# Kernel optimization log

Hardware: AMD Instinct MI355X
Metric: run time of the kernel (lower is better)

## Reference

```python
import jax, jax.numpy as jnp
import numpy as np

EPS = 1e-06
NUM_HEADS = 16
THETA = 10000.0


def rope_tables(grid_size, head_dim):
    # matches VisionRotaryEmbeddingFast: 2D rope, table shape [grid^2, head_dim]
    half = head_dim // 2
    freqs = 1.0 / THETA ** (jnp.arange(0, half, 2, dtype=jnp.float32) / half)
    freqs = jnp.concatenate([freqs, freqs], axis=0)  # [half]
    t = jnp.arange(grid_size, dtype=jnp.float32)
    f = jnp.outer(t, freqs)  # [grid, half]
    fh = jnp.broadcast_to(f[:, None, :], (grid_size, grid_size, half))
    fw = jnp.broadcast_to(f[None, :, :], (grid_size, grid_size, half))
    full = jnp.concatenate([fh, fw], axis=-1).reshape(-1, head_dim)  # [N, head_dim]
    return jnp.cos(full), jnp.sin(full)


def rotate_half(x):
    n = x.shape[-1] // 2
    return jnp.concatenate((-x[..., n:], x[..., :n]), axis=-1)


def rms_norm(x, gamma):
    var = jnp.mean(x * x, axis=-1, keepdims=True)
    return x * jax.lax.rsqrt(var + EPS) * gamma


def setup_inputs() -> dict:
    key = jax.random.key(0)
    ks = jax.random.split(key, 5)
    B, N, C = 32, 1024, 1024
    return {
        "x": jax.random.normal(ks[0], (B, N, C), dtype=jnp.float32),
        "qkv_w": jax.random.normal(ks[1], (C, 3 * C), dtype=jnp.float32) * (C ** -0.5),
        "qkv_b": jnp.zeros((3 * C,), dtype=jnp.float32),
        "proj_w": jax.random.normal(ks[2], (C, C), dtype=jnp.float32) * (C ** -0.5),
        "proj_b": jnp.zeros((C,), dtype=jnp.float32),
        "q_gamma": jnp.ones((C // NUM_HEADS,), dtype=jnp.float32),
        "k_gamma": jnp.ones((C // NUM_HEADS,), dtype=jnp.float32),
    }


def reference(x, qkv_w, qkv_b, proj_w, proj_b, q_gamma, k_gamma):
    B, N, C = x.shape
    H = NUM_HEADS
    hd = C // H
    grid = int(np.sqrt(N))
    cos, sin = rope_tables(grid, hd)  # [N, hd] each
    cos = cos[None, :, None, :]  # broadcast over [B, N, H, hd]
    sin = sin[None, :, None, :]

    qkv = (x @ qkv_w + qkv_b).reshape(B, N, 3, H, hd)
    q, k, v = qkv[:, :, 0], qkv[:, :, 1], qkv[:, :, 2]  # [B, N, H, hd]

    q = rms_norm(q, q_gamma)
    k = rms_norm(k, k_gamma)
    q = q * cos + rotate_half(q) * sin
    k = k * cos + rotate_half(k) * sin

    out = jax.nn.dot_product_attention(q, k, v, is_causal=False)  # [B, N, H, hd]
    out = out.reshape(B, N, C)
    return out @ proj_w + proj_b
```

## Files before the change

### kernel.cpp

```cpp
#include <hip/hip_runtime.h>
#include <stdint.h>

typedef float f32x4 __attribute__((ext_vector_type(4)));
typedef float f32x16 __attribute__((ext_vector_type(16)));
typedef short s16x8 __attribute__((ext_vector_type(8)));
typedef unsigned short u16;

__device__ __forceinline__ u16 f2bf(float f) {
  union { float f; uint32_t u; } c; c.f = f;
  uint32_t u = c.u;
  u = (u + 0x7fffu + ((u >> 16) & 1u)) >> 16;
  return (u16)u;
}

__device__ __forceinline__ void gload16(const void* g, void* lds) {
  __builtin_amdgcn_global_load_lds(
      (const __attribute__((address_space(1))) void*)g,
      (__attribute__((address_space(3))) void*)lds, 16, 0, 0);
}

__device__ __forceinline__ f32x4 mfma16(s16x8 a, s16x8 b, f32x4 c) {
  return __builtin_amdgcn_mfma_f32_16x16x32_bf16(a, b, c, 0, 0, 0);
}

__device__ __forceinline__ f32x16 mfma32(s16x8 a, s16x8 b, f32x16 c) {
  return __builtin_amdgcn_mfma_f32_32x32x16_bf16(a, b, c, 0, 0, 0);
}

__device__ __forceinline__ int swz(int row, int c8) {
  return row * 64 + ((c8 ^ (row & 7)) << 3);
}

__global__ void cvt_bf16(const float* __restrict__ in, u16* __restrict__ out, size_t n) {
  size_t i = ((size_t)blockIdx.x * blockDim.x + threadIdx.x) * 4;
  if (i < n) {
    float4 v = *(const float4*)&in[i];
    u16 o0 = f2bf(v.x), o1 = f2bf(v.y), o2 = f2bf(v.z), o3 = f2bf(v.w);
    uint2 packed;
    packed.x = (uint32_t)o0 | ((uint32_t)o1 << 16);
    packed.y = (uint32_t)o2 | ((uint32_t)o3 << 16);
    *(uint2*)&out[i] = packed;
  }
}

__global__ void transpose_cvt(const float* __restrict__ in, u16* __restrict__ out,
                              int rows, int cols) {
  __shared__ float tile[64][65];
  const int c0 = blockIdx.x * 64, r0 = blockIdx.y * 64;
  const int tr = threadIdx.x >> 6, tc = threadIdx.x & 63;
#pragma unroll
  for (int i = 0; i < 16; i++) {
    int r = i * 4 + tr;
    tile[r][tc] = in[(size_t)(r0 + r) * cols + c0 + tc];
  }
  __syncthreads();
#pragma unroll
  for (int i = 0; i < 16; i++) {
    int oc = i * 4 + tr;
    out[(size_t)(c0 + oc) * rows + r0 + tc] = f2bf(tile[tc][oc]);
  }
}

__global__ void rope_tables_kernel(float* __restrict__ cosT, float* __restrict__ sinT) {
  int n = blockIdx.x;
  int d = threadIdx.x;
  int ph = n >> 5, pw = n & 31;
  int pos = (d < 32) ? ph : pw;
  int fi = d & 15;
  float freq = powf(10000.f, -(float)fi / 16.f);
  float ang = (float)pos * freq;
  cosT[n * 64 + d] = cosf(ang);
  sinT[n * 64 + d] = sinf(ang);
}


#define PH_MID \
  __builtin_amdgcn_sched_barrier(0); \
  __builtin_amdgcn_s_barrier(); \
  asm volatile("s_waitcnt lgkmcnt(0)" ::: "memory"); \
  __builtin_amdgcn_sched_barrier(0); \
  __builtin_amdgcn_s_setprio(1);

#define PH_END \
  __builtin_amdgcn_s_setprio(0); \
  __builtin_amdgcn_sched_barrier(0); \
  __builtin_amdgcn_s_barrier(); \
  __builtin_amdgcn_sched_barrier(0);

#define STAGE(ldsoff, g) do { \
    gload16((g) + (size_t)(w8 + srow) * 1024 + sc8 * 8,       &lds[(ldsoff) + w8 * 64]); \
    gload16((g) + (size_t)(w8 + srow + 64) * 1024 + sc8 * 8,  &lds[(ldsoff) + (w8 + 64) * 64]); \
  } while (0)

#define RD_A(dst, BUF, mh) \
  _Pragma("unroll") \
  for (int mi = 0; mi < 4; mi++) { \
    dst[mi][0] = *(const s16x8*)&lds[(BUF) * 32768 + arow0 + ((mh) * 64 + mi * 16) * 64 + swz0]; \
    dst[mi][1] = *(const s16x8*)&lds[(BUF) * 32768 + arow0 + ((mh) * 64 + mi * 16) * 64 + swz1]; \
  }

#define RD_B(dst, BUF, nh) \
  _Pragma("unroll") \
  for (int ni = 0; ni < 2; ni++) { \
    dst[ni][0] = *(const s16x8*)&lds[(BUF) * 32768 + 16384 + brow0 + ((nh) * 32 + ni * 16) * 64 + swz0]; \
    dst[ni][1] = *(const s16x8*)&lds[(BUF) * 32768 + 16384 + brow0 + ((nh) * 32 + ni * 16) * 64 + swz1]; \
  }

#define MFMA_QUAD(af, bfr, mh, nh) \
  _Pragma("unroll") \
  for (int mi = 0; mi < 4; mi++) \
    _Pragma("unroll") \
    for (int ni = 0; ni < 2; ni++) { \
      acc[(mh) * 4 + mi][(nh) * 2 + ni] = mfma16(af[mi][0], bfr[ni][0], acc[(mh) * 4 + mi][(nh) * 2 + ni]); \
      acc[(mh) * 4 + mi][(nh) * 2 + ni] = mfma16(af[mi][1], bfr[ni][1], acc[(mh) * 4 + mi][(nh) * 2 + ni]); \
    }

#define KTILE(BUF, KT, MODE) do { \
    s16x8 a0f[4][2], a1f[4][2], b0f[2][2], b1f[2][2]; \
     \
    RD_A(a0f, BUF, 0); \
    RD_B(b0f, BUF, 0); \
    if ((MODE) < 2) STAGE((1 - (BUF)) * 32768, Ag + (size_t)((KT) + 1) * 64); \
    PH_MID; MFMA_QUAD(a0f, b0f, 0, 0); PH_END; \
     \
    RD_B(b1f, BUF, 1); \
    if ((MODE) < 2) STAGE((1 - (BUF)) * 32768 + 8192, Ag + (size_t)128 * 1024 + ((KT) + 1) * 64); \
    PH_MID; MFMA_QUAD(a0f, b1f, 0, 1); PH_END; \
     \
    RD_A(a1f, BUF, 1); \
    if ((MODE) == 0) STAGE((BUF) * 32768 + 16384, Bg + (size_t)((KT) + 2) * 64); \
    PH_MID; MFMA_QUAD(a1f, b1f, 1, 1); PH_END; \
     \
    if ((MODE) == 0) STAGE((BUF) * 32768 + 16384 + 8192, Bg + (size_t)128 * 1024 + ((KT) + 2) * 64); \
    PH_MID; MFMA_QUAD(a1f, b0f, 1, 0); \
    __builtin_amdgcn_s_setprio(0); \
    if ((MODE) == 0) asm volatile("s_waitcnt vmcnt(4)" ::: "memory"); \
    if ((MODE) == 1) asm volatile("s_waitcnt vmcnt(0)" ::: "memory"); \
    __builtin_amdgcn_sched_barrier(0); \
    __builtin_amdgcn_s_barrier(); \
    __builtin_amdgcn_sched_barrier(0); \
  } while (0)

__device__ __forceinline__ void gemm_mainloop_8ph(
    const u16* __restrict__ Ag, const u16* __restrict__ Bg,
    u16* lds, f32x4 (&acc)[8][4])
{
  const int t = threadIdx.x;
  const int l = t & 63, w = t >> 6;
  const int wm = w & 1, wn = w >> 1;
  const int lrow = l & 15, lg = l >> 4;
  const int srow = l >> 3, sc8 = (l & 7) ^ srow;
  const int w8 = w * 8;
  const int swz0 = ((0 + lg) ^ (lrow & 7)) << 3;
  const int swz1 = ((4 + lg) ^ (lrow & 7)) << 3;
  const int arow0 = (wm * 128 + lrow) * 64;
  const int brow0 = (wn * 64 + lrow) * 64;

  STAGE(0,                 Ag);
  STAGE(8192,              Ag + (size_t)128 * 1024);
  STAGE(16384,             Bg);
  STAGE(16384 + 8192,      Bg + (size_t)128 * 1024);
  STAGE(32768 + 16384,          Bg + 64);
  STAGE(32768 + 16384 + 8192,   Bg + (size_t)128 * 1024 + 64);
  asm volatile("s_waitcnt vmcnt(4)" ::: "memory");
  __builtin_amdgcn_sched_barrier(0);
  __builtin_amdgcn_s_barrier();
  __builtin_amdgcn_sched_barrier(0);

#pragma unroll 1
  for (int kt = 0; kt < 14; kt += 2) {
    KTILE(0, kt, 0);
    KTILE(1, kt + 1, 0);
  }
  KTILE(0, 14, 1);
  KTILE(1, 15, 2);
}

__global__ __launch_bounds__(512, 2) void gemm_qkv(
    const u16* __restrict__ A,
    const u16* __restrict__ Bt,
    const float* __restrict__ bias,
    const float* __restrict__ qgam, const float* __restrict__ kgam,
    const float* __restrict__ cosT, const float* __restrict__ sinT,
    u16* __restrict__ qb, u16* __restrict__ kb, u16* __restrict__ vb)
{
  __shared__ u16 lds[65536];
  const int bid = blockIdx.x;
  const int sb = (bid & 7) * 192 + (bid >> 3);
  const int bm = sb / 12, bn = sb % 12;

  const f32x4 fzero = {0.f, 0.f, 0.f, 0.f};
  f32x4 acc[8][4];
#pragma unroll
  for (int i = 0; i < 8; i++)
#pragma unroll
    for (int j = 0; j < 4; j++) acc[i][j] = fzero;

  gemm_mainloop_8ph(A + (size_t)bm * 256 * 1024, Bt + (size_t)bn * 256 * 1024, lds, acc);

  const int t = threadIdx.x, l = t & 63, w = t >> 6;
  const int wm = w & 1, wn = w >> 1, lrow = l & 15, lg = l >> 4;
  const int colb = bn * 256 + wn * 64;
  const int s = colb >> 10;
  const int h = (colb & 1023) >> 6;

  float biasv[4];
#pragma unroll
  for (int nt = 0; nt < 4; nt++) biasv[nt] = bias[colb + nt * 16 + lrow];

  if (s < 2) {
    u16* dst = (s == 0) ? qb : kb;
    const float mul = (s == 0) ? 0.18033688011112042f : 1.0f;
    const float* gamma = (s == 0) ? qgam : kgam;
    float g[4];
#pragma unroll
    for (int nt = 0; nt < 4; nt++) g[nt] = gamma[nt * 16 + lrow] * mul;
#pragma unroll
    for (int mf = 0; mf < 8; mf++) {
#pragma unroll
      for (int r = 0; r < 4; r++) {
        const int rowg = bm * 256 + wm * 128 + mf * 16 + lg * 4 + r;
        const int b = rowg >> 10, np = rowg & 1023;
        float tmp[4]; float sq = 0.f;
#pragma unroll
        for (int nt = 0; nt < 4; nt++) {
          float v = acc[mf][nt][r] + biasv[nt];
          tmp[nt] = v; sq += v * v;
        }
#pragma unroll
        for (int off = 1; off < 16; off <<= 1) sq += __shfl_xor(sq, off);
        const float rstd = rsqrtf(sq * 0.015625f + 1e-6f);
#pragma unroll
        for (int nt = 0; nt < 4; nt++) tmp[nt] *= rstd * g[nt];
        const size_t base = (((size_t)(b * 16 + h)) * 1024 + np) * 64;
#pragma unroll
        for (int nt = 0; nt < 4; nt++) {
          const int d = nt * 16 + lrow;
          const float cv = cosT[np * 64 + d], sv = sinT[np * 64 + d];
          const float rh = (nt < 2) ? -tmp[nt + 2] : tmp[nt - 2];
          dst[base + d] = f2bf(tmp[nt] * cv + rh * sv);
        }
      }
    }
  } else {
#pragma unroll
    for (int mf = 0; mf < 8; mf++) {
#pragma unroll
      for (int r = 0; r < 4; r++) {
        const int rowg = bm * 256 + wm * 128 + mf * 16 + lg * 4 + r;
        const int b = rowg >> 10, np = rowg & 1023;
        const size_t hb = ((size_t)(b * 16 + h)) * 64;
#pragma unroll
        for (int nt = 0; nt < 4; nt++) {
          const int d = nt * 16 + lrow;
          vb[(hb + d) * 1024 + np] = f2bf(acc[mf][nt][r] + biasv[nt]);
        }
      }
    }
  }
}

__global__ __launch_bounds__(256, 2) void attn_kernel(
    const u16* __restrict__ qbuf, const u16* __restrict__ kbuf,
    const u16* __restrict__ vtbuf, u16* __restrict__ obuf)
{
  __shared__ u16 Qs[256 * 64];
  __shared__ u16 Ks[2][64 * 64];
  __shared__ u16 VTs[2][64 * 64];
  __shared__ float lsumS[4][2][32];
  const int bx = blockIdx.x;
  const int xcd = bx & 7, idx = bx >> 3;
  const int bh = xcd * 64 + (idx >> 2), qt = idx & 3;
  const int t = threadIdx.x, l = t & 63, w = t >> 6;
  const int q31 = l & 31, hi = l >> 5;

  const u16* qg  = qbuf  + (size_t)bh * 65536 + (size_t)qt * 16384;
  const u16* kg0 = kbuf  + (size_t)bh * 65536;
  const u16* vt0 = vtbuf + (size_t)bh * 65536;

  const int srow = l >> 3;
  const int sc8  = (l & 7) ^ (srow & 7);

#pragma unroll
  for (int i = 0; i < 8; i++) {
    const int r0 = (w + i * 4) * 8;
    gload16(qg + (size_t)(r0 + srow) * 64 + sc8 * 8, &Qs[r0 * 64]);
  }
#pragma unroll
  for (int i = 0; i < 2; i++) {
    const int r0 = (w + i * 4) * 8;
    gload16(kg0 + (size_t)(r0 + srow) * 64 + sc8 * 8, &Ks[0][r0 * 64]);
    gload16(vt0 + (size_t)(r0 + srow) * 1024 + sc8 * 8, &VTs[0][r0 * 64]);
  }
  asm volatile("s_waitcnt vmcnt(0)" ::: "memory");
  __syncthreads();

  s16x8 bq[2][4];
#pragma unroll
  for (int qb = 0; qb < 2; qb++)
#pragma unroll
    for (int ds = 0; ds < 4; ds++)
      bq[qb][ds] = *(const s16x8*)&Qs[swz(w * 64 + qb * 32 + q31, ds * 2 + hi)];

  f32x16 o[2][2];
#pragma unroll
  for (int qb = 0; qb < 2; qb++)
#pragma unroll
    for (int kb2 = 0; kb2 < 2; kb2++)
#pragma unroll
      for (int i = 0; i < 16; i++) o[qb][kb2][i] = 0.f;
  float l_[2] = {0.f, 0.f};

#pragma unroll 2
  for (int kt = 0; kt < 16; kt++) {
    const int cur = kt & 1;
    if (kt < 15) {
      const int kb = (kt + 1) * 64;
#pragma unroll
      for (int i = 0; i < 2; i++) {
        const int r0 = (w + i * 4) * 8;
        gload16(kg0 + (size_t)(kb + r0 + srow) * 64 + sc8 * 8, &Ks[cur ^ 1][r0 * 64]);
        gload16(vt0 + (size_t)(r0 + srow) * 1024 + kb + sc8 * 8, &VTs[cur ^ 1][r0 * 64]);
      }
    }

    f32x16 s[2][2];
#pragma unroll
    for (int qb = 0; qb < 2; qb++)
#pragma unroll
      for (int kb2 = 0; kb2 < 2; kb2++)
#pragma unroll
        for (int i = 0; i < 16; i++) s[qb][kb2][i] = 0.f;
    __builtin_amdgcn_s_setprio(1);
#pragma unroll
    for (int ds = 0; ds < 4; ds++) {
      s16x8 ak0 = *(const s16x8*)&Ks[cur][swz(q31, ds * 2 + hi)];
      s16x8 ak1 = *(const s16x8*)&Ks[cur][swz(32 + q31, ds * 2 + hi)];
      s[0][0] = mfma32(ak0, bq[0][ds], s[0][0]);
      s[0][1] = mfma32(ak1, bq[0][ds], s[0][1]);
      s[1][0] = mfma32(ak0, bq[1][ds], s[1][0]);
      s[1][1] = mfma32(ak1, bq[1][ds], s[1][1]);
    }
    __builtin_amdgcn_s_setprio(0);

    s16x8 pf[2][4];
#pragma unroll
    for (int qb = 0; qb < 2; qb++) {
      float p[32];
#pragma unroll
      for (int r = 0; r < 16; r++) p[r] = __builtin_amdgcn_exp2f(s[qb][0][r]);
#pragma unroll
      for (int r = 0; r < 16; r++) p[16 + r] = __builtin_amdgcn_exp2f(s[qb][1][r]);
      {
        float sm0 = 0.f, sm1 = 0.f, sm2 = 0.f, sm3 = 0.f;
#pragma unroll
        for (int r = 0; r < 8; r++) {
          sm0 += p[r]; sm1 += p[8 + r]; sm2 += p[16 + r]; sm3 += p[24 + r];
        }
        l_[qb] += (sm0 + sm1) + (sm2 + sm3);
      }
#pragma unroll
      for (int j = 0; j < 4; j++) {
        uint32_t a1, b1, a2, b2;
        asm("v_cvt_pk_bf16_f32 %0, %1, %2" : "=v"(a1) : "v"(p[j * 8 + 0]), "v"(p[j * 8 + 1]));
        asm("v_cvt_pk_bf16_f32 %0, %1, %2" : "=v"(b1) : "v"(p[j * 8 + 2]), "v"(p[j * 8 + 3]));
        asm("v_cvt_pk_bf16_f32 %0, %1, %2" : "=v"(a2) : "v"(p[j * 8 + 4]), "v"(p[j * 8 + 5]));
        asm("v_cvt_pk_bf16_f32 %0, %1, %2" : "=v"(b2) : "v"(p[j * 8 + 6]), "v"(p[j * 8 + 7]));
        asm("v_permlane32_swap_b32 %0, %1" : "+v"(a1), "+v"(a2));
        asm("v_permlane32_swap_b32 %0, %1" : "+v"(b1), "+v"(b2));
        union { s16x8 v; uint32_t u[4]; } cvt;
        cvt.u[0] = a1; cvt.u[1] = b1; cvt.u[2] = a2; cvt.u[3] = b2;
        pf[qb][j] = cvt.v;
      }
    }

    __builtin_amdgcn_s_setprio(1);
#pragma unroll
    for (int j = 0; j < 4; j++) {
      s16x8 bv0 = *(const s16x8*)&VTs[cur][swz(q31, j * 2 + hi)];
      s16x8 bv1 = *(const s16x8*)&VTs[cur][swz(32 + q31, j * 2 + hi)];
      o[0][0] = mfma32(pf[0][j], bv0, o[0][0]);
      o[0][1] = mfma32(pf[0][j], bv1, o[0][1]);
      o[1][0] = mfma32(pf[1][j], bv0, o[1][0]);
      o[1][1] = mfma32(pf[1][j], bv1, o[1][1]);
    }
    __builtin_amdgcn_s_setprio(0);

    __syncthreads();
  }

#pragma unroll
  for (int qb = 0; qb < 2; qb++) {
    l_[qb] += __shfl_xor(l_[qb], 32);
    if (l < 32) lsumS[w][qb][q31] = 1.0f / l_[qb];
  }

  const int b = bh >> 4, h = bh & 15;
#pragma unroll
  for (int qb = 0; qb < 2; qb++)
#pragma unroll
    for (int r = 0; r < 16; r++) {
      const int q = (r & 3) + 8 * (r >> 2) + 4 * hi;
      const float inv = lsumS[w][qb][q];
      const int n = qt * 256 + w * 64 + qb * 32 + q;
      const size_t base = (((size_t)b * 1024 + n) * 16 + h) * 64;
      obuf[base + q31]      = f2bf(o[qb][0][r] * inv);
      obuf[base + 32 + q31] = f2bf(o[qb][1][r] * inv);
    }
}

__global__ __launch_bounds__(512, 2) void gemm_proj(
    const u16* __restrict__ A,
    const u16* __restrict__ Bt,
    const float* __restrict__ bias,
    float* __restrict__ out)
{
  __shared__ u16 lds[65536];
  const int bid = blockIdx.x;
  const int sb = (bid & 7) * 64 + (bid >> 3);
  const int bm = sb >> 2, bn = sb & 3;

  const f32x4 fzero = {0.f, 0.f, 0.f, 0.f};
  f32x4 acc[8][4];
#pragma unroll
  for (int i = 0; i < 8; i++)
#pragma unroll
    for (int j = 0; j < 4; j++) acc[i][j] = fzero;

  gemm_mainloop_8ph(A + (size_t)bm * 256 * 1024, Bt + (size_t)bn * 256 * 1024, lds, acc);

  const int t = threadIdx.x, l = t & 63, w = t >> 6;
  const int wm = w & 1, wn = w >> 1, lrow = l & 15, lg = l >> 4;
  const int colb = bn * 256 + wn * 64;
  float biasv[4];
#pragma unroll
  for (int nt = 0; nt < 4; nt++) biasv[nt] = bias[colb + nt * 16 + lrow];

#pragma unroll
  for (int mf = 0; mf < 8; mf++) {
#pragma unroll
    for (int r = 0; r < 4; r++) {
      const int rowg = bm * 256 + wm * 128 + mf * 16 + lg * 4 + r;
#pragma unroll
      for (int nt = 0; nt < 4; nt++) {
        const int col = colb + nt * 16 + lrow;
        out[(size_t)rowg * 1024 + col] = acc[mf][nt][r] + biasv[nt];
      }
    }
  }
}

extern "C" void kernel_launch(void* const* d_in, const int* in_sizes, int n_in,
                              void* d_out, int out_size, void* d_ws, size_t ws_size,
                              hipStream_t stream) {
  const float* x      = (const float*)d_in[0];
  const float* qkv_w  = (const float*)d_in[1];
  const float* qkv_b  = (const float*)d_in[2];
  const float* proj_w = (const float*)d_in[3];
  const float* proj_b = (const float*)d_in[4];
  const float* q_gam  = (const float*)d_in[5];
  const float* k_gam  = (const float*)d_in[6];

  char* ws = (char*)d_ws;
  u16*   xb   = (u16*)(ws);
  u16*   qb   = (u16*)(ws + 67108864);
  u16*   kb   = (u16*)(ws + 134217728);
  u16*   vb   = (u16*)(ws + 201326592);
  u16*   wqT  = (u16*)(ws + 268435456);
  u16*   wpT  = (u16*)(ws + 274726912);
  float* cosT = (float*)(ws + 276824064);
  float* sinT = (float*)(ws + 277086208);
  u16*   attn = xb;

  cvt_bf16<<<32768, 256, 0, stream>>>(x, xb, (size_t)33554432);
  transpose_cvt<<<dim3(48, 16), 256, 0, stream>>>(qkv_w, wqT, 1024, 3072);
  transpose_cvt<<<dim3(16, 16), 256, 0, stream>>>(proj_w, wpT, 1024, 1024);
  rope_tables_kernel<<<1024, 64, 0, stream>>>(cosT, sinT);

  gemm_qkv<<<dim3(1536), dim3(512), 0, stream>>>(xb, wqT, qkv_b, q_gam, k_gam,
                                                 cosT, sinT, qb, kb, vb);
  attn_kernel<<<2048, 256, 0, stream>>>(qb, kb, vb, attn);
  gemm_proj<<<dim3(512), dim3(512), 0, stream>>>(attn, wpT, proj_b, (float*)d_out);
}
```

Before: 685.1 us.

## Raise attention occupancy by dropping Q LDS tile and splitting KV tile in halves

```diff
diff --git a/kernel.cpp b/kernel.cpp
--- a/kernel.cpp
+++ b/kernel.cpp
@@ -260,11 +260,10 @@
   }
 }
 
-__global__ __launch_bounds__(256, 2) void attn_kernel(
+__global__ __launch_bounds__(256, 3) void attn_kernel(
     const u16* __restrict__ qbuf, const u16* __restrict__ kbuf,
     const u16* __restrict__ vtbuf, u16* __restrict__ obuf)
 {
-  __shared__ u16 Qs[256 * 64];
   __shared__ u16 Ks[2][64 * 64];
   __shared__ u16 VTs[2][64 * 64];
   __shared__ float lsumS[4][2][32];
@@ -282,26 +281,22 @@
   const int sc8  = (l & 7) ^ (srow & 7);
 
 #pragma unroll
-  for (int i = 0; i < 8; i++) {
-    const int r0 = (w + i * 4) * 8;
-    gload16(qg + (size_t)(r0 + srow) * 64 + sc8 * 8, &Qs[r0 * 64]);
-  }
-#pragma unroll
   for (int i = 0; i < 2; i++) {
     const int r0 = (w + i * 4) * 8;
     gload16(kg0 + (size_t)(r0 + srow) * 64 + sc8 * 8, &Ks[0][r0 * 64]);
     gload16(vt0 + (size_t)(r0 + srow) * 1024 + sc8 * 8, &VTs[0][r0 * 64]);
   }
+
+  s16x8 bq[2][4];
+#pragma unroll
+  for (int qb = 0; qb < 2; qb++)
+#pragma unroll
+    for (int ds = 0; ds < 4; ds++)
+      bq[qb][ds] = *(const s16x8*)&qg[(w * 64 + qb * 32 + q31) * 64 + ds * 16 + hi * 8];
+
   asm volatile("s_waitcnt vmcnt(0)" ::: "memory");
   __syncthreads();
 
-  s16x8 bq[2][4];
-#pragma unroll
-  for (int qb = 0; qb < 2; qb++)
-#pragma unroll
-    for (int ds = 0; ds < 4; ds++)
-      bq[qb][ds] = *(const s16x8*)&Qs[swz(w * 64 + qb * 32 + q31, ds * 2 + hi)];
-
   f32x16 o[2][2];
 #pragma unroll
   for (int qb = 0; qb < 2; qb++)
@@ -311,7 +306,6 @@
       for (int i = 0; i < 16; i++) o[qb][kb2][i] = 0.f;
   float l_[2] = {0.f, 0.f};
 
-#pragma unroll 2
   for (int kt = 0; kt < 16; kt++) {
     const int cur = kt & 1;
     if (kt < 15) {
@@ -324,67 +318,61 @@
       }
     }
 
-    f32x16 s[2][2];
-#pragma unroll
-    for (int qb = 0; qb < 2; qb++)
-#pragma unroll
-      for (int kb2 = 0; kb2 < 2; kb2++)
-#pragma unroll
-        for (int i = 0; i < 16; i++) s[qb][kb2][i] = 0.f;
-    __builtin_amdgcn_s_setprio(1);
-#pragma unroll
-    for (int ds = 0; ds < 4; ds++) {
-      s16x8 ak0 = *(const s16x8*)&Ks[cur][swz(q31, ds * 2 + hi)];
-      s16x8 ak1 = *(const s16x8*)&Ks[cur][swz(32 + q31, ds * 2 + hi)];
-      s[0][0] = mfma32(ak0, bq[0][ds], s[0][0]);
-      s[0][1] = mfma32(ak1, bq[0][ds], s[0][1]);
-      s[1][0] = mfma32(ak0, bq[1][ds], s[1][0]);
-      s[1][1] = mfma32(ak1, bq[1][ds], s[1][1]);
-    }
-    __builtin_amdgcn_s_setprio(0);
-
-    s16x8 pf[2][4];
-#pragma unroll
-    for (int qb = 0; qb < 2; qb++) {
-      float p[32];
-#pragma unroll
-      for (int r = 0; r < 16; r++) p[r] = __builtin_amdgcn_exp2f(s[qb][0][r]);
-#pragma unroll
-      for (int r = 0; r < 16; r++) p[16 + r] = __builtin_amdgcn_exp2f(s[qb][1][r]);
-      {
-        float sm0 = 0.f, sm1 = 0.f, sm2 = 0.f, sm3 = 0.f;
-#pragma unroll
-        for (int r = 0; r < 8; r++) {
-          sm0 += p[r]; sm1 += p[8 + r]; sm2 += p[16 + r]; sm3 += p[24 + r];
+#pragma unroll
+    for (int kbh = 0; kbh < 2; kbh++) {
+      f32x16 s0, s1;
+#pragma unroll
+      for (int i = 0; i < 16; i++) { s0[i] = 0.f; s1[i] = 0.f; }
+      __builtin_amdgcn_s_setprio(1);
+#pragma unroll
+      for (int ds = 0; ds < 4; ds++) {
+        s16x8 ak = *(const s16x8*)&Ks[cur][swz(kbh * 32 + q31, ds * 2 + hi)];
+        s0 = mfma32(ak, bq[0][ds], s0);
+        s1 = mfma32(ak, bq[1][ds], s1);
+      }
+      __builtin_amdgcn_s_setprio(0);
+
+      s16x8 pf[2][2];
+#pragma unroll
+      for (int qb = 0; qb < 2; qb++) {
+        float p[16];
+#pragma unroll
+        for (int r = 0; r < 16; r++)
+          p[r] = __builtin_amdgcn_exp2f(qb == 0 ? s0[r] : s1[r]);
+        {
+          float sm0 = 0.f, sm1 = 0.f;
+#pragma unroll
+          for (int r = 0; r < 8; r++) { sm0 += p[r]; sm1 += p[8 + r]; }
+          l_[qb] += sm0 + sm1;
         }
-        l_[qb] += (sm0 + sm1) + (sm2 + sm3);
-      }
-#pragma unroll
-      for (int j = 0; j < 4; j++) {
-        uint32_t a1, b1, a2, b2;
-        asm("v_cvt_pk_bf16_f32 %0, %1, %2" : "=v"(a1) : "v"(p[j * 8 + 0]), "v"(p[j * 8 + 1]));
-        asm("v_cvt_pk_bf16_f32 %0, %1, %2" : "=v"(b1) : "v"(p[j * 8 + 2]), "v"(p[j * 8 + 3]));
-        asm("v_cvt_pk_bf16_f32 %0, %1, %2" : "=v"(a2) : "v"(p[j * 8 + 4]), "v"(p[j * 8 + 5]));
-        asm("v_cvt_pk_bf16_f32 %0, %1, %2" : "=v"(b2) : "v"(p[j * 8 + 6]), "v"(p[j * 8 + 7]));
-        asm("v_permlane32_swap_b32 %0, %1" : "+v"(a1), "+v"(a2));
-        asm("v_permlane32_swap_b32 %0, %1" : "+v"(b1), "+v"(b2));
-        union { s16x8 v; uint32_t u[4]; } cvt;
-        cvt.u[0] = a1; cvt.u[1] = b1; cvt.u[2] = a2; cvt.u[3] = b2;
-        pf[qb][j] = cvt.v;
-      }
-    }
-
-    __builtin_amdgcn_s_setprio(1);
-#pragma unroll
-    for (int j = 0; j < 4; j++) {
-      s16x8 bv0 = *(const s16x8*)&VTs[cur][swz(q31, j * 2 + hi)];
-      s16x8 bv1 = *(const s16x8*)&VTs[cur][swz(32 + q31, j * 2 + hi)];
-      o[0][0] = mfma32(pf[0][j], bv0, o[0][0]);
-      o[0][1] = mfma32(pf[0][j], bv1, o[0][1]);
-      o[1][0] = mfma32(pf[1][j], bv0, o[1][0]);
-      o[1][1] = mfma32(pf[1][j], bv1, o[1][1]);
-    }
-    __builtin_amdgcn_s_setprio(0);
+#pragma unroll
+        for (int jj = 0; jj < 2; jj++) {
+          uint32_t a1, b1, a2, b2;
+          asm("v_cvt_pk_bf16_f32 %0, %1, %2" : "=v"(a1) : "v"(p[jj * 8 + 0]), "v"(p[jj * 8 + 1]));
+          asm("v_cvt_pk_bf16_f32 %0, %1, %2" : "=v"(b1) : "v"(p[jj * 8 + 2]), "v"(p[jj * 8 + 3]));
+          asm("v_cvt_pk_bf16_f32 %0, %1, %2" : "=v"(a2) : "v"(p[jj * 8 + 4]), "v"(p[jj * 8 + 5]));
+          asm("v_cvt_pk_bf16_f32 %0, %1, %2" : "=v"(b2) : "v"(p[jj * 8 + 6]), "v"(p[jj * 8 + 7]));
+          asm("v_permlane32_swap_b32 %0, %1" : "+v"(a1), "+v"(a2));
+          asm("v_permlane32_swap_b32 %0, %1" : "+v"(b1), "+v"(b2));
+          union { s16x8 v; uint32_t u[4]; } cvt;
+          cvt.u[0] = a1; cvt.u[1] = b1; cvt.u[2] = a2; cvt.u[3] = b2;
+          pf[qb][jj] = cvt.v;
+        }
+      }
+
+      __builtin_amdgcn_s_setprio(1);
+#pragma unroll
+      for (int jj = 0; jj < 2; jj++) {
+        const int j = kbh * 2 + jj;
+        s16x8 bv0 = *(const s16x8*)&VTs[cur][swz(q31, j * 2 + hi)];
+        s16x8 bv1 = *(const s16x8*)&VTs[cur][swz(32 + q31, j * 2 + hi)];
+        o[0][0] = mfma32(pf[0][jj], bv0, o[0][0]);
+        o[0][1] = mfma32(pf[0][jj], bv1, o[0][1]);
+        o[1][0] = mfma32(pf[1][jj], bv0, o[1][0]);
+        o[1][1] = mfma32(pf[1][jj], bv1, o[1][1]);
+      }
+      __builtin_amdgcn_s_setprio(0);
+    }
 
     __syncthreads();
   }
```

Measured after the change: 724.2 us. 1.06x slower.
